# Performance work log

Hardware: AMD Instinct MI355X
Metric: run time of the kernel (lower is better)

Reference implementation:

```python
import jax, jax.numpy as jnp
import numpy as np

QMIN, QMAX = 0.0, 255.0
# activation statistics (min, max) per layer, from init_kwargs['stats']
STATS = {"conv1": (-0.5, 3.0), "conv2": (0.0, 6.0), "fc1": (0.0, 8.0), "fc2": (0.0, 10.0)}


def calc_scale_zp(min_val, max_val):
    scale = (max_val - min_val) / (QMAX - QMIN)
    # original: int(clamped initial zero point) -> truncation
    zp = jnp.trunc(jnp.clip(QMIN - min_val / scale, QMIN, QMAX))
    return scale, zp


def quantize(x, min_val=None, max_val=None):
    if min_val is None:
        min_val, max_val = x.min(), x.max()
    scale, zp = calc_scale_zp(min_val, max_val)
    q = jnp.round(jnp.clip(zp + x / scale, QMIN, QMAX))
    return q, scale, zp


def conv2d(x, w, b):
    y = jax.lax.conv_general_dilated(x, w, (1, 1), "VALID",
                                     dimension_numbers=("NCHW", "OIHW", "NCHW"))
    return y + b[None, :, None, None]


def linear(x, w, b):
    return x @ w.T + b


def max_pool_2x2(x):
    return jax.lax.reduce_window(x, -jnp.inf, jax.lax.max, (1, 1, 2, 2), (1, 1, 2, 2), "VALID")


def quantize_layer(q_x, scale_x, zp_x, W, B, apply_fn, stat):
    # fake-quant weights/bias with their own min/max
    wq, scale_w, zp_w = quantize(W)
    bq, scale_b, zp_b = quantize(B)
    scale_next, zp_next = calc_scale_zp(stat[0], stat[1])
    X = q_x - zp_x
    W_eff = scale_x * scale_w * (wq - zp_w)
    B_eff = scale_b * (bq + zp_b)  # '+ zp_b' is faithful to the source
    y = jax.nn.relu(apply_fn(X, W_eff, B_eff) / scale_next + zp_next)
    # .round().byte() in torch wraps mod 256
    return jnp.mod(jnp.round(y), 256.0), scale_next, zp_next


def setup_inputs() -> dict:
    key = jax.random.key(0)
    ks = jax.random.split(key, 9)
    B = 4096
    return {
        "x": jax.random.normal(ks[0], (B, 1, 28, 28), jnp.float32),
        "conv1_w": jax.random.normal(ks[1], (20, 1, 5, 5), jnp.float32) * 0.1,
        "conv1_b": jax.random.normal(ks[2], (20,), jnp.float32) * 0.1,
        "conv2_w": jax.random.normal(ks[3], (50, 20, 5, 5), jnp.float32) * 0.05,
        "conv2_b": jax.random.normal(ks[4], (50,), jnp.float32) * 0.05,
        "fc1_w": jax.random.normal(ks[5], (500, 800), jnp.float32) * 0.03,
        "fc1_b": jax.random.normal(ks[6], (500,), jnp.float32) * 0.03,
        "fc2_w": jax.random.normal(ks[7], (10, 500), jnp.float32) * 0.05,
        "fc2_b": jax.random.normal(ks[8], (10,), jnp.float32) * 0.05,
    }


def reference(x, conv1_w, conv1_b, conv2_w, conv2_b, fc1_w, fc1_b, fc2_w, fc2_b):
    q, s, zp = quantize(x, STATS["conv1"][0], STATS["conv1"][1])
    q, s, zp = quantize_layer(q, s, zp, conv1_w, conv1_b, conv2d, STATS["conv2"])
    q = max_pool_2x2(q)                       # [B,20,12,12]
    q, s, zp = quantize_layer(q, s, zp, conv2_w, conv2_b, conv2d, STATS["fc1"])
    q = max_pool_2x2(q)                       # [B,50,4,4]
    q = q.reshape(-1, 4 * 4 * 50)             # [B,800]
    q, s, zp = quantize_layer(q, s, zp, fc1_w, fc1_b, linear, STATS["fc2"])
    xf = s * (q - zp)                         # dequantize
    logits = linear(xf, fc2_w, fc2_b)         # [B,10]
    return jax.nn.log_softmax(logits, axis=1)
```

## Files before the change

### kernel.cpp

```cpp
#include <hip/hip_runtime.h>
#include <cmath>

#define TPB 256
typedef float floatx4 __attribute__((ext_vector_type(4)));
typedef __bf16 bf16x8 __attribute__((ext_vector_type(8)));
typedef unsigned short ushort8 __attribute__((ext_vector_type(8)));
typedef unsigned short ushort_t;

#define OFF_PMN 16
#define OFF_PMX 96
#define OFF_B1 520
#define OFF_B2 544
#define OFF_B3 600
#define W1BF_BYTE 6144
#define W2BF_BYTE 8192
#define W3BF_BYTE 131072
#define PART_BYTE 1048576
#define Q2_BYTE  29360128ULL

#define S_X1 (3.5f/255.0f)
#define ZP_X1 36.0f
#define S_N1 (6.0f/255.0f)
#define S_N2 (8.0f/255.0f)
#define S_N3 (10.0f/255.0f)

#define XSTR 40
#define NCG 4

__device__ inline float qclip(float x, float s, float zp){
    return rintf(fminf(fmaxf(zp + x / s, 0.0f), 255.0f));
}
__device__ inline ushort_t bfbits(float v){
    return (ushort_t)(__float_as_uint(v) >> 16);
}

__global__ __launch_bounds__(TPB) void k_minmax(
        const float* c1w, const float* c1b, const float* c2w, const float* c2b,
        const float* f1w, const float* f1b, float* pmn, float* pmx){
    __shared__ float smn[TPB], smx[TPB];
    int bb = blockIdx.x, tid = threadIdx.x;
    const float* src; int n, sub, nsub;
    if      (bb == 0){ src=c1w; n=500;    sub=0;     nsub=1;  }
    else if (bb == 1){ src=c1b; n=20;     sub=0;     nsub=1;  }
    else if (bb <  6){ src=c2w; n=25000;  sub=bb-2;  nsub=4;  }
    else if (bb == 6){ src=c2b; n=50;     sub=0;     nsub=1;  }
    else if (bb < 71){ src=f1w; n=400000; sub=bb-7;  nsub=64; }
    else             { src=f1b; n=500;    sub=0;     nsub=1;  }
    float mn = INFINITY, mx = -INFINITY;
    for (int i = sub*TPB + tid; i < n; i += nsub*TPB){
        float v = src[i]; mn = fminf(mn, v); mx = fmaxf(mx, v);
    }
    smn[tid] = mn; smx[tid] = mx; __syncthreads();
    for (int s = TPB/2; s > 0; s >>= 1){
        if (tid < s){
            smn[tid] = fminf(smn[tid], smn[tid+s]);
            smx[tid] = fmaxf(smx[tid], smx[tid+s]);
        }
        __syncthreads();
    }
    if (tid == 0){ pmn[bb] = smn[0]; pmx[bb] = smx[0]; }
}

#define N_EFF 452157
__global__ __launch_bounds__(TPB) void k_make_eff(
        const float* c1w, const float* c1b, const float* c2w, const float* c2b,
        const float* f1w, const float* f1b, const float* pmn, const float* pmx,
        float* ws, ushort_t* w1bf, ushort_t* w2bf, ushort_t* w3bf){
    __shared__ float sS[6], sZ[6];
    int tid = threadIdx.x;
    int wv = tid >> 6, lane = tid & 63;
    const int starts[6] = {0,1,2,6,7,71};
    const int counts[6] = {1,1,4,1,64,1};
    #pragma unroll
    for (int rep = 0; rep < 2; ++rep){
        int t = wv + rep*4;
        if (t < 6){
            float mn = INFINITY, mx = -INFINITY;
            if (lane < counts[t]){ mn = pmn[starts[t]+lane]; mx = pmx[starts[t]+lane]; }
            #pragma unroll
            for (int off = 32; off > 0; off >>= 1){
                mn = fminf(mn, __shfl_xor(mn, off));
                mx = fmaxf(mx, __shfl_xor(mx, off));
            }
            if (lane == 0){
                float s = (mx - mn) / 255.0f;
                sS[t] = s;
                sZ[t] = truncf(fminf(fmaxf(0.0f - mn / s, 0.0f), 255.0f));
            }
        }
    }
    __syncthreads();

    int i = blockIdx.x * TPB + tid;
    if (i >= N_EFF) return;
    if (i < 1024){
        int n = i >> 5, k = i & 31;
        float v = 0.0f;
        if (n < 20 && k < 25) v = qclip(c1w[n*25 + k], sS[0], sZ[0]) - sZ[0];
        w1bf[i] = bfbits(v);
    } else if (i < 1044){
        int j = i - 1024;
        ws[OFF_B1 + j] = (sS[1] * (qclip(c1b[j], sS[1], sZ[1]) + sZ[1])) / S_N1;
    } else if (i < 42004){
        int j = i - 1044;
        int c = j >> 11, r = j & 2047, co = r >> 5, k = r & 31;
        int q = k >> 3, jj = k & 7;
        int tap, ci; bool valid;
        if (c < 13){ tap = 2*c + (q>>1); ci = (q&1)*8 + jj; valid = (tap < 25); }
        else       { tap = 4*(c-13) + q; ci = 16 + jj;      valid = (tap < 25) && (jj < 4); }
        valid = valid && (co < 50);
        float v = 0.0f;
        if (valid) v = qclip(c2w[(co*20 + ci)*25 + tap], sS[2], sZ[2]) - sZ[2];
        w2bf[j] = bfbits(v);
    } else if (i < 42054){
        int j = i - 42004;
        ws[OFF_B2 + j] = (sS[3] * (qclip(c2b[j], sS[3], sZ[3]) + sZ[3])) / S_N2;
    } else if (i < 451654){
        int j = i - 42054;
        int n = j / 800, k = j - 800*n;
        float v = 0.0f;
        if (n < 500) v = qclip(f1w[n*800 + k], sS[4], sZ[4]) - sZ[4];
        w3bf[j] = bfbits(v);
    } else if (i < 452154){
        int j = i - 451654;
        ws[OFF_B3 + j] = (sS[5] * (qclip(f1b[j], sS[5], sZ[5]) + sZ[5])) / S_N3;
    } else if (i == 452154){
        ws[0] = (S_N1 * sS[2]) / S_N2;
    } else if (i == 452155){
        ws[1] = (S_N2 * sS[4]) / S_N3;
    } else {
        ws[2] = (S_X1 * sS[0]) / S_N1;
    }
}

__global__ __launch_bounds__(TPB) void k_conv12(const float* x, const ushort_t* w1bf,
                                                const ushort_t* w2bt, const float* ws,
                                                ushort_t* q2bf, int B){
    __shared__ __align__(16) ushort_t xs[144*XSTR];
    __shared__ __align__(16) ushort_t xim[3136];
    int b = blockIdx.x, tid = threadIdx.x;
    int lane = tid & 63, wv = tid >> 6;
    int ln = lane & 15, quad = lane >> 4;

    for (int i = tid; i < 144; i += TPB){
        *(unsigned int*)(xs + i*XSTR + 20) = 0u;
        *(unsigned int*)(xs + i*XSTR + 22) = 0u;
    }

    const float* xb = x + (size_t)b * 784;
    for (int i = tid; i < 784; i += TPB){
        float v = xb[i];
        float q = rintf(fminf(fmaxf(ZP_X1 + v / S_X1, 0.0f), 255.0f));
        ushort_t bits = bfbits(q - ZP_X1);
        xim[i] = bits; xim[784 + i] = bits; xim[1568 + i] = bits; xim[2352 + i] = bits;
    }

    int offj[8];
    #pragma unroll
    for (int j = 0; j < 8; ++j){
        int k = quad*8 + j;
        int kh = k / 5, kw = k - 5*kh;
        offj[j] = (k < 25) ? (kh*28 + kw) : 0;
    }
    const ushort_t* xq = xim + quad*784;

    ushort8 bw0 = *(const ushort8*)(w1bf + ln*32 + quad*8);
    ushort8 bw1 = *(const ushort8*)(w1bf + (16 + ln)*32 + quad*8);
    bf16x8 bf0 = __builtin_bit_cast(bf16x8, bw0);
    bf16x8 bf1 = __builtin_bit_cast(bf16x8, bw1);

    float K1 = ws[2];
    float B1_0 = ws[OFF_B1 + ln];
    float B1_1 = (ln < 4) ? ws[OFF_B1 + 16 + ln] : 0.0f;
    __syncthreads();

    for (int i = 0; i < 9; ++i){
        int mt = 9*wv + i;
        int m = mt*16 + ln;
        int p = m >> 2, crn = m & 3;
        int ph_ = p / 12, pw_ = p - 12*ph_;
        int oh = 2*ph_ + (crn >> 1), ow = 2*pw_ + (crn & 1);
        int base = oh*28 + ow;
        ushort8 aw;
        #pragma unroll
        for (int j = 0; j < 8; ++j)
            aw[j] = xq[base + offj[j]];
        bf16x8 af = __builtin_bit_cast(bf16x8, aw);
        floatx4 z = (floatx4){0.f,0.f,0.f,0.f};
        floatx4 a0 = __builtin_amdgcn_mfma_f32_16x16x32_bf16(af, bf0, z, 0, 0, 0);
        floatx4 a1 = __builtin_amdgcn_mfma_f32_16x16x32_bf16(af, bf1, z, 0, 0, 0);

        int pp = mt*4 + quad;
        {
            float y0 = fmaf(a0[0], K1, B1_0), y1 = fmaf(a0[1], K1, B1_0);
            float y2 = fmaf(a0[2], K1, B1_0), y3 = fmaf(a0[3], K1, B1_0);
            float mA = fmaxf(fmaxf(y0, y1), y2);
            float mf = fmaxf(fmaxf(mA, y3), 0.0f);
            if (__ballot(mf >= 255.5f)){
                unsigned int q0 = ((unsigned int)rintf(fmaxf(y0,0.f))) & 255u;
                unsigned int q1 = ((unsigned int)rintf(fmaxf(y1,0.f))) & 255u;
                unsigned int qq2 = ((unsigned int)rintf(fmaxf(y2,0.f))) & 255u;
                unsigned int q3 = ((unsigned int)rintf(fmaxf(y3,0.f))) & 255u;
                unsigned int h0 = q0 > q1 ? q0 : q1;
                unsigned int h1 = qq2 > q3 ? qq2 : q3;
                mf = (float)(h0 > h1 ? h0 : h1);
            } else {
                mf = rintf(mf);
            }
            xs[pp*XSTR + ln] = bfbits(mf);
        }
        if (ln < 4){
            float y0 = fmaf(a1[0], K1, B1_1), y1 = fmaf(a1[1], K1, B1_1);
            float y2 = fmaf(a1[2], K1, B1_1), y3 = fmaf(a1[3], K1, B1_1);
            float mA = fmaxf(fmaxf(y0, y1), y2);
            float mf = fmaxf(fmaxf(mA, y3), 0.0f);
            if (__ballot(mf >= 255.5f)){
                unsigned int q0 = ((unsigned int)rintf(fmaxf(y0,0.f))) & 255u;
                unsigned int q1 = ((unsigned int)rintf(fmaxf(y1,0.f))) & 255u;
                unsigned int qq2 = ((unsigned int)rintf(fmaxf(y2,0.f))) & 255u;
                unsigned int q3 = ((unsigned int)rintf(fmaxf(y3,0.f))) & 255u;
                unsigned int h0 = q0 > q1 ? q0 : q1;
                unsigned int h1 = qq2 > q3 ? qq2 : q3;
                mf = (float)(h0 > h1 ? h0 : h1);
            } else {
                mf = rintf(mf);
            }
            xs[pp*XSTR + 16 + ln] = bfbits(mf);
        }
    }
    __syncthreads();

    int mt0 = (wv & 1) * 2;
    int nt0 = (wv >> 1) * 2;
    int abase[2];
    #pragma unroll
    for (int mi = 0; mi < 2; ++mi)
        abase[mi] = (24*(mt0+mi) + (ln>>3)*12 + (ln&7)) * XSTR;
    int aoff[20];
    #pragma unroll
    for (int c = 0; c < 20; ++c){
        int tap, inner;
        if (c < 13){ tap = 2*c + (quad>>1); inner = (quad&1)*8; }
        else       { tap = 4*(c-13) + quad; inner = 16; }
        int pt = 0;
        if (tap < 25){ int kh = tap/5, kw = tap-5*kh; pt = kh*12 + kw; }
        aoff[c] = pt*XSTR + inner;
    }

    float sc2d = ws[0];
    const ushort_t* bsrc0 = w2bt + (size_t)(nt0*16 + ln)*32 + quad*8;
    const ushort_t* bsrc1 = bsrc0 + 16*32;

    floatx4 acc[2][2];
    #pragma unroll
    for (int mi = 0; mi < 2; ++mi)
        #pragma unroll
        for (int ni = 0; ni < 2; ++ni) acc[mi][ni] = (floatx4){0.f,0.f,0.f,0.f};

    #pragma unroll
    for (int c = 0; c < 20; ++c){
        ushort8 b0w = *(const ushort8*)(bsrc0 + c*2048);
        ushort8 b1w = *(const ushort8*)(bsrc1 + c*2048);
        ushort8 a0w = *(const ushort8*)(xs + abase[0] + aoff[c]);
        ushort8 a1w = *(const ushort8*)(xs + abase[1] + aoff[c]);
        bf16x8 a0 = __builtin_bit_cast(bf16x8, a0w);
        bf16x8 a1 = __builtin_bit_cast(bf16x8, a1w);
        bf16x8 b0 = __builtin_bit_cast(bf16x8, b0w);
        bf16x8 b1 = __builtin_bit_cast(bf16x8, b1w);
        acc[0][0] = __builtin_amdgcn_mfma_f32_16x16x32_bf16(a0, b0, acc[0][0], 0, 0, 0);
        acc[0][1] = __builtin_amdgcn_mfma_f32_16x16x32_bf16(a0, b1, acc[0][1], 0, 0, 0);
        acc[1][0] = __builtin_amdgcn_mfma_f32_16x16x32_bf16(a1, b0, acc[1][0], 0, 0, 0);
        acc[1][1] = __builtin_amdgcn_mfma_f32_16x16x32_bf16(a1, b1, acc[1][1], 0, 0, 0);
    }

    #pragma unroll
    for (int ni = 0; ni < 2; ++ni){
        int co = (nt0 + ni)*16 + ln;
        float bias2d = (co < 50) ? ws[OFF_B2 + co] : 0.0f;
        #pragma unroll
        for (int mi = 0; mi < 2; ++mi){
            int mt = mt0 + mi;
            float y0 = fmaf(acc[mi][ni][0], sc2d, bias2d);
            float y1 = fmaf(acc[mi][ni][1], sc2d, bias2d);
            float y2 = fmaf(acc[mi][ni][2], sc2d, bias2d);
            float y3 = fmaf(acc[mi][ni][3], sc2d, bias2d);
            float f0 = fmaxf(fmaxf(y0, y1), 0.0f);
            float f1 = fmaxf(fmaxf(y2, y3), 0.0f);
            float g0 = __shfl_xor(f0, 32);
            float g1 = __shfl_xor(f1, 32);
            float v0f = fmaxf(f0, g0), v1f = fmaxf(f1, g1);
            if (__ballot(fmaxf(v0f, v1f) >= 255.5f)){
                unsigned int q0 = ((unsigned int)rintf(fmaxf(y0,0.f))) & 255u;
                unsigned int q1 = ((unsigned int)rintf(fmaxf(y1,0.f))) & 255u;
                unsigned int qq2 = ((unsigned int)rintf(fmaxf(y2,0.f))) & 255u;
                unsigned int q3 = ((unsigned int)rintf(fmaxf(y3,0.f))) & 255u;
                unsigned int h0 = q0 > q1 ? q0 : q1;
                unsigned int h1 = qq2 > q3 ? qq2 : q3;
                unsigned int p0 = (unsigned int)__shfl_xor((int)h0, 32);
                unsigned int p1 = (unsigned int)__shfl_xor((int)h1, 32);
                v0f = (float)(h0 > p0 ? h0 : p0);
                v1f = (float)(h1 > p1 ? h1 : p1);
            } else {
                v0f = rintf(v0f); v1f = rintf(v1f);
            }
            if (quad < 2 && co < 50){
                size_t base = (size_t)b*800 + co*16 + mt*4 + quad*2;
                q2bf[base]     = bfbits(v0f);
                q2bf[base + 1] = bfbits(v1f);
            }
        }
    }
}

__global__ __launch_bounds__(256) void k_fc12(const ushort_t* q2bf, const ushort_t* w3bf,
                                              const float* ws, const float* w2,
                                              float* part, int B){
    __shared__ float red[4*16*10];
    int tid = threadIdx.x;
    int lane = tid & 63, wv = tid >> 6;
    int ln = lane & 15, quad = lane >> 4;
    int bi = blockIdx.x;
    int cg = bi & (NCG-1);
    int b0 = (bi >> 2) * 16;
    int n0 = cg*128 + wv*32;

    const ushort_t* asrc = q2bf + (size_t)(b0 + ln)*800 + quad*8;
    const ushort_t* bsrc = w3bf + (size_t)(n0 + ln)*800 + quad*8;

    floatx4 acc[2];
    acc[0] = (floatx4){0.f,0.f,0.f,0.f};
    acc[1] = (floatx4){0.f,0.f,0.f,0.f};

    for (int c = 0; c < 25; ++c){
        ushort8 aw = *(const ushort8*)(asrc + c*32);
        bf16x8 af = __builtin_bit_cast(bf16x8, aw);
        ushort8 b0w = *(const ushort8*)(bsrc + c*32);
        ushort8 b1w = *(const ushort8*)(bsrc + 16*800 + c*32);
        acc[0] = __builtin_amdgcn_mfma_f32_16x16x32_bf16(
                     af, __builtin_bit_cast(bf16x8, b0w), acc[0], 0, 0, 0);
        acc[1] = __builtin_amdgcn_mfma_f32_16x16x32_bf16(
                     af, __builtin_bit_cast(bf16x8, b1w), acc[1], 0, 0, 0);
    }

    float sc3d = ws[1];
    float xf[4][2];
    #pragma unroll
    for (int t = 0; t < 2; ++t){
        int col = n0 + t*16 + ln;
        float bias = (col < 500) ? ws[OFF_B3 + col] : 0.0f;
        #pragma unroll
        for (int r = 0; r < 4; ++r){
            float y = fmaxf(fmaf(acc[t][r], sc3d, bias), 0.0f);
            unsigned int q = ((unsigned int)rintf(y)) & 255u;
            xf[r][t] = (col < 500) ? S_N3 * (float)q : 0.0f;
        }
    }

    #pragma unroll
    for (int c = 0; c < 10; ++c){
        float p[4] = {0.f, 0.f, 0.f, 0.f};
        #pragma unroll
        for (int t = 0; t < 2; ++t){
            int col = n0 + t*16 + ln;
            float w = (col < 500) ? w2[c*500 + col] : 0.0f;
            #pragma unroll
            for (int r = 0; r < 4; ++r) p[r] = fmaf(xf[r][t], w, p[r]);
        }
        #pragma unroll
        for (int m = 1; m <= 8; m <<= 1)
            #pragma unroll
            for (int r = 0; r < 4; ++r) p[r] += __shfl_xor(p[r], m);
        if (ln == 0){
            #pragma unroll
            for (int r = 0; r < 4; ++r)
                red[(wv*16 + quad*4 + r)*10 + c] = p[r];
        }
    }
    __syncthreads();

    if (tid < 160){
        int row = tid / 10, c = tid - 10*(tid/10);
        float s = red[row*10 + c] + red[160 + row*10 + c]
                + red[320 + row*10 + c] + red[480 + row*10 + c];
        part[((size_t)cg*B + b0 + row)*10 + c] = s;
    }
}

__global__ __launch_bounds__(256) void k_softmax(const float* part, const float* b2,
                                                 float* out, int B){
    int i = blockIdx.x*256 + threadIdx.x;
    if (i >= B) return;
    float lg[10], mx = -INFINITY;
    #pragma unroll
    for (int c = 0; c < 10; ++c){
        float s = b2[c];
        #pragma unroll
        for (int g = 0; g < NCG; ++g) s += part[((size_t)g*B + i)*10 + c];
        lg[c] = s; mx = fmaxf(mx, s);
    }
    float sum = 0.0f;
    #pragma unroll
    for (int c = 0; c < 10; ++c) sum += expf(lg[c] - mx);
    float ls = logf(sum);
    #pragma unroll
    for (int c = 0; c < 10; ++c)
        out[(size_t)i*10 + c] = lg[c] - mx - ls;
}

extern "C" void kernel_launch(void* const* d_in, const int* in_sizes, int n_in,
                              void* d_out, int out_size, void* d_ws, size_t ws_size,
                              hipStream_t stream){
    const float* x   = (const float*)d_in[0];
    const float* c1w = (const float*)d_in[1];
    const float* c1b = (const float*)d_in[2];
    const float* c2w = (const float*)d_in[3];
    const float* c2b = (const float*)d_in[4];
    const float* f1w = (const float*)d_in[5];
    const float* f1b = (const float*)d_in[6];
    const float* f2w = (const float*)d_in[7];
    const float* f2b = (const float*)d_in[8];
    int B = in_sizes[0] / 784;

    float* ws = (float*)d_ws;
    float* pmn = ws + OFF_PMN;
    float* pmx = ws + OFF_PMX;
    ushort_t* w1bf = (ushort_t*)((char*)d_ws + W1BF_BYTE);
    ushort_t* w2bf = (ushort_t*)((char*)d_ws + W2BF_BYTE);
    ushort_t* w3bf = (ushort_t*)((char*)d_ws + W3BF_BYTE);
    float* part = (float*)((char*)d_ws + PART_BYTE);
    ushort_t* q2bf = (ushort_t*)((char*)d_ws + Q2_BYTE);
    float* out = (float*)d_out;

    k_minmax<<<72, TPB, 0, stream>>>(c1w, c1b, c2w, c2b, f1w, f1b, pmn, pmx);
    k_make_eff<<<(N_EFF + TPB - 1)/TPB, TPB, 0, stream>>>(c1w, c1b, c2w, c2b, f1w, f1b, pmn, pmx, ws, w1bf, w2bf, w3bf);
    k_conv12<<<B, TPB, 0, stream>>>(x, w1bf, w2bf, ws, q2bf, B);
    k_fc12<<<(B/16)*NCG, 256, 0, stream>>>(q2bf, w3bf, ws, f2w, part, B);
    k_softmax<<<(B + 255)/256, 256, 0, stream>>>(part, f2b, out, B);
}
```

Measured before the change: 160.4 us.

## Pack conv1 im2col input as bf16 pairs and prefetch fc1 operands

Conv1's shared-memory input is stored as packed pairs of adjacent bf16 pixels, and the conv1 weight K layout is remapped (TAPOF) so each lane gathers four 32-bit words instead of eight 16-bit loads. The input is also loaded as float4 vectors. The fc1 MFMA loop is fully unrolled with register double-buffering of the A/B fragments, and conv12 gets a launch-bounds occupancy hint. The aim is to cut LDS gather instructions and hide global load latency, at the cost of more registers and a padded weight layout that must stay consistent between kernels.

After: 164.0 us. 2.2% more time.

```diff
diff --git a/kernel.cpp b/kernel.cpp
--- a/kernel.cpp
+++ b/kernel.cpp
@@ -5,6 +5,8 @@
 typedef float floatx4 __attribute__((ext_vector_type(4)));
 typedef __bf16 bf16x8 __attribute__((ext_vector_type(8)));
 typedef unsigned short ushort8 __attribute__((ext_vector_type(8)));
+typedef unsigned int uintx4 __attribute__((ext_vector_type(4)));
+typedef unsigned int uint2v __attribute__((ext_vector_type(2)));
 typedef unsigned short ushort_t;
 
 #define OFF_PMN 16
@@ -26,6 +28,20 @@
 
 #define XSTR 40
 #define NCG 4
+#define PSTR 792
+
+__device__ const signed char TAPOF[32] = {
+     0,  1,  2,  3,  4, -1,  5,  6,
+     7,  8,  9, -1, 10, 11, 12, 13,
+    14, -1, 15, 16, 17, 18, 19, -1,
+    20, 21, 22, 23, 24, -1, -1, -1
+};
+__device__ const int OFFP[4][4] = {
+    {0, 2, 4, 28},
+    {30, 32, 56, 58},
+    {60, 84, 86, 88},
+    {112, 114, 116, 112}
+};
 
 __device__ inline float qclip(float x, float s, float zp){
     return rintf(fminf(fmaxf(zp + x / s, 0.0f), 255.0f));
@@ -95,8 +111,9 @@
     if (i >= N_EFF) return;
     if (i < 1024){
         int n = i >> 5, k = i & 31;
+        int tap = (int)TAPOF[k];
         float v = 0.0f;
-        if (n < 20 && k < 25) v = qclip(c1w[n*25 + k], sS[0], sZ[0]) - sZ[0];
+        if (n < 20 && tap >= 0) v = qclip(c1w[n*25 + tap], sS[0], sZ[0]) - sZ[0];
         w1bf[i] = bfbits(v);
     } else if (i < 1044){
         int j = i - 1024;
@@ -133,11 +150,11 @@
     }
 }
 
-__global__ __launch_bounds__(TPB) void k_conv12(const float* x, const ushort_t* w1bf,
-                                                const ushort_t* w2bt, const float* ws,
-                                                ushort_t* q2bf, int B){
+__global__ __launch_bounds__(TPB, 4) void k_conv12(const float* x, const ushort_t* w1bf,
+                                                   const ushort_t* w2bt, const float* ws,
+                                                   ushort_t* q2bf, int B){
     __shared__ __align__(16) ushort_t xs[144*XSTR];
-    __shared__ __align__(16) ushort_t xim[3136];
+    __shared__ __align__(16) unsigned int ximp[4*PSTR];
     int b = blockIdx.x, tid = threadIdx.x;
     int lane = tid & 63, wv = tid >> 6;
     int ln = lane & 15, quad = lane >> 4;
@@ -148,21 +165,25 @@
     }
 
     const float* xb = x + (size_t)b * 784;
-    for (int i = tid; i < 784; i += TPB){
-        float v = xb[i];
-        float q = rintf(fminf(fmaxf(ZP_X1 + v / S_X1, 0.0f), 255.0f));
-        ushort_t bits = bfbits(q - ZP_X1);
-        xim[i] = bits; xim[784 + i] = bits; xim[1568 + i] = bits; xim[2352 + i] = bits;
-    }
-
-    int offj[8];
-    #pragma unroll
-    for (int j = 0; j < 8; ++j){
-        int k = quad*8 + j;
-        int kh = k / 5, kw = k - 5*kh;
-        offj[j] = (k < 25) ? (kh*28 + kw) : 0;
-    }
-    const ushort_t* xq = xim + quad*784;
+    if (tid < 196){
+        floatx4 v = *(const floatx4*)(xb + tid*4);
+        float x5 = (tid < 195) ? xb[tid*4 + 4] : 0.0f;
+        ushort_t bq[5];
+        #pragma unroll
+        for (int j = 0; j < 4; ++j)
+            bq[j] = bfbits(rintf(fminf(fmaxf(ZP_X1 + v[j] / S_X1, 0.0f), 255.0f)) - ZP_X1);
+        bq[4] = bfbits(rintf(fminf(fmaxf(ZP_X1 + x5 / S_X1, 0.0f), 255.0f)) - ZP_X1);
+        uintx4 P;
+        #pragma unroll
+        for (int j = 0; j < 4; ++j)
+            P[j] = (unsigned int)bq[j] | ((unsigned int)bq[j+1] << 16);
+        #pragma unroll
+        for (int c = 0; c < 4; ++c)
+            *(uintx4*)(ximp + c*PSTR + tid*4) = P;
+    }
+
+    const unsigned int* xp = ximp + quad*PSTR;
+    int o0 = OFFP[quad][0], o1 = OFFP[quad][1], o2 = OFFP[quad][2], o3 = OFFP[quad][3];
 
     ushort8 bw0 = *(const ushort8*)(w1bf + ln*32 + quad*8);
     ushort8 bw1 = *(const ushort8*)(w1bf + (16 + ln)*32 + quad*8);
@@ -181,11 +202,12 @@
         int ph_ = p / 12, pw_ = p - 12*ph_;
         int oh = 2*ph_ + (crn >> 1), ow = 2*pw_ + (crn & 1);
         int base = oh*28 + ow;
-        ushort8 aw;
-        #pragma unroll
-        for (int j = 0; j < 8; ++j)
-            aw[j] = xq[base + offj[j]];
-        bf16x8 af = __builtin_bit_cast(bf16x8, aw);
+        uintx4 pv;
+        pv[0] = xp[base + o0];
+        pv[1] = xp[base + o1];
+        pv[2] = xp[base + o2];
+        pv[3] = xp[base + o3];
+        bf16x8 af = __builtin_bit_cast(bf16x8, pv);
         floatx4 z = (floatx4){0.f,0.f,0.f,0.f};
         floatx4 a0 = __builtin_amdgcn_mfma_f32_16x16x32_bf16(af, bf0, z, 0, 0, 0);
         floatx4 a1 = __builtin_amdgcn_mfma_f32_16x16x32_bf16(af, bf1, z, 0, 0, 0);
@@ -325,21 +347,31 @@
     int n0 = cg*128 + wv*32;
 
     const ushort_t* asrc = q2bf + (size_t)(b0 + ln)*800 + quad*8;
-    const ushort_t* bsrc = w3bf + (size_t)(n0 + ln)*800 + quad*8;
+    const ushort_t* bsrc0 = w3bf + (size_t)(n0 + ln)*800 + quad*8;
+    const ushort_t* bsrc1 = bsrc0 + 16*800;
 
     floatx4 acc[2];
     acc[0] = (floatx4){0.f,0.f,0.f,0.f};
     acc[1] = (floatx4){0.f,0.f,0.f,0.f};
 
+    ushort8 aw  = *(const ushort8*)(asrc);
+    ushort8 b0w = *(const ushort8*)(bsrc0);
+    ushort8 b1w = *(const ushort8*)(bsrc1);
+    #pragma unroll
     for (int c = 0; c < 25; ++c){
-        ushort8 aw = *(const ushort8*)(asrc + c*32);
-        bf16x8 af = __builtin_bit_cast(bf16x8, aw);
-        ushort8 b0w = *(const ushort8*)(bsrc + c*32);
-        ushort8 b1w = *(const ushort8*)(bsrc + 16*800 + c*32);
+        ushort8 aN, b0N, b1N;
+        if (c < 24){
+            aN  = *(const ushort8*)(asrc  + (c+1)*32);
+            b0N = *(const ushort8*)(bsrc0 + (c+1)*32);
+            b1N = *(const ushort8*)(bsrc1 + (c+1)*32);
+        }
         acc[0] = __builtin_amdgcn_mfma_f32_16x16x32_bf16(
-                     af, __builtin_bit_cast(bf16x8, b0w), acc[0], 0, 0, 0);
+                     __builtin_bit_cast(bf16x8, aw), __builtin_bit_cast(bf16x8, b0w),
+                     acc[0], 0, 0, 0);
         acc[1] = __builtin_amdgcn_mfma_f32_16x16x32_bf16(
-                     af, __builtin_bit_cast(bf16x8, b1w), acc[1], 0, 0, 0);
+                     __builtin_bit_cast(bf16x8, aw), __builtin_bit_cast(bf16x8, b1w),
+                     acc[1], 0, 0, 0);
+        aw = aN; b0w = b0N; b1w = b1N;
     }
 
     float sc3d = ws[1];
```
